# Kernel tuning notes

Hardware: AMD Instinct MI355X
Metric: run time of the kernel (lower is better)

Reference implementation:

```python
import jax, jax.numpy as jnp
import numpy as np

GROUPS = 8
EPS = 1e-5


def setup_inputs() -> dict:
    key = jax.random.key(0)
    ks = jax.random.split(key, 7)
    b, c, h, w = 32, 256, 32, 32
    x = jax.random.normal(ks[0], (b, c, h, w), dtype=jnp.float32)
    gn_weight = jax.random.normal(ks[1], (c,), dtype=jnp.float32) * 0.02 + 1.0
    gn_bias = jax.random.normal(ks[2], (c,), dtype=jnp.float32) * 0.02
    w_qkv = jax.random.normal(ks[3], (3 * c, c), dtype=jnp.float32) / np.sqrt(c)
    b_qkv = jax.random.normal(ks[4], (3 * c,), dtype=jnp.float32) * 0.01
    w_out = jax.random.normal(ks[5], (c, c), dtype=jnp.float32) / np.sqrt(c)
    b_out = jax.random.normal(ks[6], (c,), dtype=jnp.float32) * 0.01
    return {"x": x, "gn_weight": gn_weight, "gn_bias": gn_bias,
            "w_qkv": w_qkv, "b_qkv": b_qkv, "w_out": w_out, "b_out": b_out}


def group_norm(x, weight, bias):
    b, c, h, w = x.shape
    xg = x.reshape(b, GROUPS, c // GROUPS, h, w)
    mean = jnp.mean(xg, axis=(2, 3, 4), keepdims=True)
    var = jnp.var(xg, axis=(2, 3, 4), keepdims=True)
    xg = (xg - mean) * jax.lax.rsqrt(var + EPS)
    x = xg.reshape(b, c, h, w)
    return x * weight[None, :, None, None] + bias[None, :, None, None]


def reference(x, gn_weight, gn_bias, w_qkv, b_qkv, w_out, b_out):
    b, c, h, w = x.shape
    x_norm = group_norm(x, gn_weight, gn_bias)
    # 1x1 conv == channel matmul: (b, 3c, h, w)
    qkv = jnp.einsum('oc,bchw->bohw', w_qkv, x_norm) + b_qkv[None, :, None, None]
    q, k, v = jnp.split(qkv, 3, axis=1)
    hw = h * w
    q = q.reshape(b, c, hw)  # used transposed: (b, hw, c)
    k = k.reshape(b, c, hw)
    v = v.reshape(b, c, hw)
    scale = 1.0 / jnp.sqrt(jnp.float32(c))
    attn = jax.nn.softmax(jnp.einsum('bcs,bct->bst', q, k) * scale, axis=-1)  # (b, hw, hw)
    out = jnp.einsum('bst,bct->bcs', attn, v).reshape(b, c, h, w)
    out = jnp.einsum('oc,bchw->bohw', w_out, out) + b_out[None, :, None, None]
    return out + x
```

## Files before the change

kernel.cpp:

```cpp
#include <hip/hip_runtime.h>
#include <hip/hip_bf16.h>


typedef __bf16 bf16x8 __attribute__((ext_vector_type(8)));
typedef __bf16 bf16x4 __attribute__((ext_vector_type(4)));
typedef float f32x4 __attribute__((ext_vector_type(4)));
typedef float f32x16 __attribute__((ext_vector_type(16)));

#define MFMA16(a, b, c) __builtin_amdgcn_mfma_f32_16x16x32_bf16(a, b, c, 0, 0, 0)
#define MFMA32(a, b, c) __builtin_amdgcn_mfma_f32_32x32x16_bf16(a, b, c, 0, 0, 0)

#define GLD16(gsrc_, ldst_)                                                                  \
    __builtin_amdgcn_global_load_lds((const __attribute__((address_space(1))) void*)(gsrc_), \
                                     (__attribute__((address_space(3))) void*)(ldst_), 16, 0, 0)

__global__ __launch_bounds__(256) void gn_stats(const float* __restrict__ x,
                                                float* __restrict__ stats,
                                                const float* __restrict__ wqkv,
                                                const float* __restrict__ wout,
                                                __bf16* __restrict__ wbf) {
    const int bid = blockIdx.x, t = threadIdx.x;
    if (bid < 128) {
        int idx = (bid * 256 + t) * 8;
        const float* src = (idx < 196608) ? (wqkv + idx) : (wout + (idx - 196608));
        float4 v0 = *(const float4*)src;
        float4 v1 = *(const float4*)(src + 4);
        bf16x8 o;
        o[0] = (__bf16)v0.x; o[1] = (__bf16)v0.y; o[2] = (__bf16)v0.z; o[3] = (__bf16)v0.w;
        o[4] = (__bf16)v1.x; o[5] = (__bf16)v1.y; o[6] = (__bf16)v1.z; o[7] = (__bf16)v1.w;
        *(bf16x8*)&wbf[idx] = o;
    }
    const int bg = bid >> 3, part = bid & 7;
    const float* xp = x + (size_t)bg * 32768 + part * 4096;
    float s = 0.f, s2 = 0.f;
    #pragma unroll
    for (int i = 0; i < 4; i++) {
        float4 v = *(const float4*)(xp + (i * 256 + t) * 4);
        s  += v.x + v.y + v.z + v.w;
        s2 += v.x*v.x + v.y*v.y + v.z*v.z + v.w*v.w;
    }
    #pragma unroll
    for (int o = 32; o > 0; o >>= 1) { s += __shfl_down(s, o, 64); s2 += __shfl_down(s2, o, 64); }
    __shared__ float red[8];
    const int wv = t >> 6;
    if ((t & 63) == 0) { red[wv * 2] = s; red[wv * 2 + 1] = s2; }
    __syncthreads();
    if (t == 0) {
        float ts  = red[0] + red[2] + red[4] + red[6];
        float ts2 = red[1] + red[3] + red[5] + red[7];
        stats[bg * 16 + part * 2]     = ts;
        stats[bg * 16 + part * 2 + 1] = ts2;
    }
}

__global__ __launch_bounds__(512) void gn_apply(const float* __restrict__ x,
                                                const float* __restrict__ stats,
                                                const float* __restrict__ gw,
                                                const float* __restrict__ gb,
                                                __bf16* __restrict__ xnT) {
    const int bid = blockIdx.x;
    const int bg = bid >> 3, part = bid & 7;
    const int b = bg >> 3, g = bg & 7;
    const int t = threadIdx.x;
    float ts = 0.f, ts2 = 0.f;
    #pragma unroll
    for (int p = 0; p < 8; p++) { ts += stats[bg * 16 + p * 2]; ts2 += stats[bg * 16 + p * 2 + 1]; }
    const float mean = ts / 32768.f;
    const float inv = rsqrtf(ts2 / 32768.f - mean * mean + 1e-5f);
    __shared__ __bf16 Lds[32][136];
    const int c = t >> 4, ss = (t & 15) * 8;
    const float ga = gw[g * 32 + c], be = gb[g * 32 + c];
    const float* xp = x + (((size_t)b * 256 + g * 32 + c) * 1024) + part * 128 + ss;
    float4 v0 = *(const float4*)xp;
    float4 v1 = *(const float4*)(xp + 4);
    float vv[8] = {v0.x, v0.y, v0.z, v0.w, v1.x, v1.y, v1.z, v1.w};
    bf16x8 wv;
    #pragma unroll
    for (int i = 0; i < 8; i++) wv[i] = (__bf16)((vv[i] - mean) * inv * ga + be);
    *(bf16x8*)&Lds[c][ss] = wv;
    __syncthreads();
    const int row = t >> 2, cb = (t & 3) * 8;
    bf16x8 ov;
    #pragma unroll
    for (int j = 0; j < 8; j++) ov[j] = Lds[cb + j][row];
    *(bf16x8*)&xnT[((size_t)b * 1024 + part * 128 + row) * 256 + g * 32 + cb] = ov;
}

#define GEMM64P_BODY(ArowBase_, BrowBase_)                                              \
    f32x4 acc[4][4] = {};                                                               \
    {                                                                                   \
        _Pragma("unroll")                                                               \
        for (int i = 0; i < 4; i++) {                                                   \
            const int ch = wave * 4 + i;                                                \
            const int r = ch * 8 + (lane >> 3);                                         \
            const int sw = ((lane & 7) ^ (r & 7)) * 8;                                  \
            GLD16((ArowBase_) + (size_t)r * 256 + sw, (char*)&As[0][0][0] + ch * 1024); \
            GLD16((BrowBase_) + (size_t)r * 256 + sw, (char*)&Bs[0][0][0] + ch * 1024); \
        }                                                                               \
    }                                                                                   \
    _Pragma("unroll")                                                                   \
    for (int kk = 0; kk < 4; kk++) {                                                    \
        if (kk < 3) {                                                                   \
            _Pragma("unroll")                                                           \
            for (int i = 0; i < 4; i++) {                                               \
                const int ch = wave * 4 + i;                                            \
                const int r = ch * 8 + (lane >> 3);                                     \
                const int sw = ((lane & 7) ^ (r & 7)) * 8;                              \
                GLD16((ArowBase_) + (size_t)r * 256 + (kk + 1) * 64 + sw,               \
                      (char*)&As[(kk + 1) & 1][0][0] + ch * 1024);                      \
                GLD16((BrowBase_) + (size_t)r * 256 + (kk + 1) * 64 + sw,               \
                      (char*)&Bs[(kk + 1) & 1][0][0] + ch * 1024);                      \
            }                                                                           \
            asm volatile("s_waitcnt vmcnt(8)" ::: "memory");                            \
        } else {                                                                        \
            asm volatile("s_waitcnt vmcnt(0)" ::: "memory");                            \
        }                                                                               \
        asm volatile("s_barrier" ::: "memory");                                         \
        _Pragma("unroll")                                                               \
        for (int kh = 0; kh < 2; kh++) {                                                \
            bf16x8 af[4], bfv[4];                                                       \
            _Pragma("unroll")                                                           \
            for (int im = 0; im < 4; im++) {                                            \
                const int row = wm + im * 16 + l16;                                     \
                af[im] = *(const bf16x8*)&As[kk & 1][row][(((kh * 4 + quad) ^ (row & 7)) * 8)]; \
            }                                                                           \
            _Pragma("unroll")                                                           \
            for (int in = 0; in < 4; in++) {                                            \
                const int row = wn + in * 16 + l16;                                     \
                bfv[in] = *(const bf16x8*)&Bs[kk & 1][row][(((kh * 4 + quad) ^ (row & 7)) * 8)]; \
            }                                                                           \
            _Pragma("unroll")                                                           \
            for (int im = 0; im < 4; im++)                                              \
                _Pragma("unroll")                                                       \
                for (int in = 0; in < 4; in++)                                          \
                    acc[im][in] = MFMA16(af[im], bfv[in], acc[im][in]);                 \
        }                                                                               \
        asm volatile("s_waitcnt lgkmcnt(0)" ::: "memory");                              \
        asm volatile("s_barrier" ::: "memory");                                        \
    }

__global__ __launch_bounds__(256) void qkv_gemm(const __bf16* __restrict__ wbf,
                                                const float* __restrict__ bias,
                                                const __bf16* __restrict__ xnT,
                                                __bf16* __restrict__ qtr,
                                                __bf16* __restrict__ ktr,
                                                __bf16* __restrict__ vbuf) {
    __shared__ union {
        struct { __bf16 A[2][128][64]; __bf16 B[2][128][64]; } g;
        __bf16 ct[128][136];
    } sm;
    const int lin = blockIdx.x + ((blockIdx.y + blockIdx.z * 6) << 3);
    const int xcd = lin & 7, idx = lin >> 3;
    const int gwk = xcd * 192 + idx;
    const int mt = gwk % 6, panel = gwk / 6;
    const int b = panel >> 3;
    const int n0 = (panel & 7) * 128, m0 = mt * 128;
    const int t = threadIdx.x;
    const int wave = t >> 6, lane = t & 63, quad = lane >> 4, l16 = lane & 15;
    const int wm = (wave & 1) * 64, wn = (wave >> 1) * 64;
    const __bf16* arow = wbf + (size_t)m0 * 256;
    const __bf16* brow = xnT + ((size_t)b * 1024 + n0) * 256;
    auto As = sm.g.A;
    auto Bs = sm.g.B;

    GEMM64P_BODY(arow, brow)

    if (m0 < 512) {
        #pragma unroll
        for (int im = 0; im < 4; im++) {
            #pragma unroll
            for (int in = 0; in < 4; in++) {
                int ob = m0 + wm + im * 16 + quad * 4;
                bf16x4 ov;
                #pragma unroll
                for (int r = 0; r < 4; r++) ov[r] = (__bf16)(acc[im][in][r] + bias[ob + r]);
                *(bf16x4*)&sm.ct[wn + in * 16 + l16][wm + im * 16 + quad * 4] = ov;
            }
        }
        __syncthreads();
        {
            const int rbase = t >> 2, cf = t & 3;
            #pragma unroll
            for (int rr = 0; rr < 2; rr++) {
                int row = rbase + rr * 64;
                int sg = n0 + row;
                __bf16* dst = (m0 < 256) ? &qtr[((size_t)b * 1024 + sg) * 256 + m0]
                                         : &ktr[((size_t)b * 1024 + sg) * 256 + (m0 - 256)];
                #pragma unroll
                for (int u = 0; u < 4; u++) {
                    int colb = cf * 8 + u * 32;
                    *(bf16x8*)&dst[colb] = *(const bf16x8*)&sm.ct[row][colb];
                }
            }
        }
    } else {
        #pragma unroll
        for (int im = 0; im < 4; im++) {
            #pragma unroll
            for (int in = 0; in < 4; in++) {
                int cl = wm + im * 16 + quad * 4;
                int tl = wn + in * 16 + l16;
                #pragma unroll
                for (int r = 0; r < 4; r++)
                    sm.ct[cl + r][tl] = (__bf16)(acc[im][in][r] + bias[m0 + cl + r]);
            }
        }
        __syncthreads();
        {
            const int row = t >> 1, tc = (t & 1) * 64;
            const int cglob = m0 - 512 + row;
            __bf16* dst = &vbuf[((size_t)b * 256 + cglob) * 1024 + n0 + tc];
            #pragma unroll
            for (int u = 0; u < 8; u++)
                *(bf16x8*)&dst[u * 8] = *(const bf16x8*)&sm.ct[row][tc + u * 8];
        }
    }
}

__global__ __launch_bounds__(512, 2) void attn_kernel(const __bf16* __restrict__ qtr,
                                                      const __bf16* __restrict__ ktr,
                                                      const __bf16* __restrict__ vbuf,
                                                      __bf16* __restrict__ aoT) {
    __shared__ __bf16 Kt[2][32][260];
    __shared__ __bf16 Vs[2][256][36];
    __shared__ bf16x8 Pl[4][2][2][64];
    __shared__ float Lred[4][2][32];
    const int b = blockIdx.x;
    const int tid = threadIdx.x;
    const int wave = tid >> 6, lane = tid & 63, half = lane >> 5, l31 = lane & 31;
    const int pair = wave & 3, th = wave >> 2;
    const int s0 = blockIdx.y * 128 + pair * 32;
    const float kscale = 0.09016844f;

    bf16x8 aq[16];
    #pragma unroll
    for (int ks = 0; ks < 16; ks++)
        aq[ks] = *(const bf16x8*)&qtr[((size_t)b * 1024 + s0 + l31) * 256 + ks * 16 + half * 8];

    const int k_row = tid >> 3;
    const int k_cb  = (tid & 7) * 8;
    const int v_c   = tid >> 1;
    const int v_th  = tid & 1;
    const size_t kbase = (size_t)b * 1024 * 256;
    const size_t vbase = (size_t)b * 256 * 1024;

    float l_acc = 0.f;
    f32x16 o_acc[4] = {};

    bf16x8 kpre[4], vpre[4];
    #pragma unroll
    for (int u = 0; u < 4; u++) {
        kpre[u] = *(const bf16x8*)&ktr[kbase + (size_t)k_row * 256 + k_cb + u * 64];
        vpre[u] = *(const bf16x8*)&vbuf[vbase + (size_t)v_c * 1024 + v_th * 32 + u * 8];
    }

    for (int it = 0; it < 16; it++) {
        #pragma unroll
        for (int u = 0; u < 4; u++)
            *(bf16x8*)&Kt[k_row >> 5][k_row & 31][k_cb + u * 64] = kpre[u];
        #pragma unroll
        for (int u = 0; u < 4; u++) {
            const bf16x4* hv = (const bf16x4*)&vpre[u];
            const int sbase = (u >> 1) * 16 + (u & 1) * 4;
            *(bf16x4*)&Vs[v_th][v_c][sbase]     = hv[0];
            *(bf16x4*)&Vs[v_th][v_c][sbase + 8] = hv[1];
        }
        __syncthreads();
        if (it < 15) {
            const int t1 = (it + 1) * 64;
            #pragma unroll
            for (int u = 0; u < 4; u++) {
                kpre[u] = *(const bf16x8*)&ktr[kbase + (size_t)(t1 + k_row) * 256 + k_cb + u * 64];
                vpre[u] = *(const bf16x8*)&vbuf[vbase + (size_t)v_c * 1024 + t1 + v_th * 32 + u * 8];
            }
        }

        f32x16 sc_a = {}, sc_b = {};
        __builtin_amdgcn_s_setprio(1);
        #pragma unroll
        for (int ks = 0; ks < 8; ks++) {
            bf16x8 bk0 = *(const bf16x8*)&Kt[th][l31][ks * 16 + half * 8];
            bf16x8 bk1 = *(const bf16x8*)&Kt[th][l31][(ks + 8) * 16 + half * 8];
            sc_a = MFMA32(bk0, aq[ks], sc_a);
            sc_b = MFMA32(bk1, aq[ks + 8], sc_b);
        }
        __builtin_amdgcn_s_setprio(0);

        bf16x8 pf0, pf1;
        #pragma unroll
        for (int r = 0; r < 8; r++) {
            float p = exp2f((sc_a[r] + sc_b[r]) * kscale);
            l_acc += p;
            pf0[r] = (__bf16)p;
        }
        #pragma unroll
        for (int r = 8; r < 16; r++) {
            float p = exp2f((sc_a[r] + sc_b[r]) * kscale);
            l_acc += p;
            pf1[r - 8] = (__bf16)p;
        }
        Pl[pair][th][0][lane] = pf0;
        Pl[pair][th][1][lane] = pf1;
        __syncthreads();
        bf16x8 pp0 = Pl[pair][1 - th][0][lane];
        bf16x8 pp1 = Pl[pair][1 - th][1][lane];

        bf16x8 ap[4];
        if (th == 0) { ap[0] = pf0; ap[1] = pf1; ap[2] = pp0; ap[3] = pp1; }
        else         { ap[0] = pp0; ap[1] = pp1; ap[2] = pf0; ap[3] = pf1; }

        __builtin_amdgcn_s_setprio(1);
        #pragma unroll
        for (int n = 0; n < 4; n++) {
            int c = th * 128 + n * 32 + l31;
            #pragma unroll
            for (int kc = 0; kc < 4; kc++) {
                bf16x8 bv = *(const bf16x8*)&Vs[kc >> 1][c][(kc & 1) * 16 + half * 8];
                o_acc[n] = MFMA32(ap[kc], bv, o_acc[n]);
            }
        }
        __builtin_amdgcn_s_setprio(0);
        __syncthreads();
    }

    l_acc += __shfl_xor(l_acc, 32, 64);
    if (lane < 32) Lred[pair][th][l31] = l_acc;
    __syncthreads();
    #pragma unroll
    for (int r = 0; r < 16; r++) {
        int row = (r & 3) + 8 * (r >> 2) + 4 * half;
        float rinv = 1.0f / (Lred[pair][0][row] + Lred[pair][1][row]);
        #pragma unroll
        for (int n = 0; n < 4; n++) {
            int c = th * 128 + n * 32 + l31;
            aoT[((size_t)b * 1024 + s0 + row) * 256 + c] = (__bf16)(o_acc[n][r] * rinv);
        }
    }
}

__global__ __launch_bounds__(256) void proj_gemm(const __bf16* __restrict__ wbf_out,
                                                 const float* __restrict__ bias,
                                                 const __bf16* __restrict__ aoT,
                                                 const float* __restrict__ resid,
                                                 float* __restrict__ Out) {
    __shared__ union {
        struct { __bf16 A[2][128][64]; __bf16 B[2][128][64]; } g;
        float cf[64][132];
    } sm;
    const int lin = blockIdx.x + ((blockIdx.y + blockIdx.z * 2) << 3);
    const int xcd = lin & 7, idx = lin >> 3;
    const int gwk = xcd * 64 + idx;
    const int mt = gwk & 1, panel = gwk >> 1;
    const int b = panel >> 3;
    const int n0 = (panel & 7) * 128, m0 = mt * 128;
    const int t = threadIdx.x;
    const int wave = t >> 6, lane = t & 63, quad = lane >> 4, l16 = lane & 15;
    const int wm = (wave & 1) * 64, wn = (wave >> 1) * 64;
    const __bf16* arow = wbf_out + (size_t)m0 * 256;
    const __bf16* brow = aoT + ((size_t)b * 1024 + n0) * 256;
    auto As = sm.g.A;
    auto Bs = sm.g.B;

    GEMM64P_BODY(arow, brow)

    for (int h = 0; h < 2; h++) {
        if ((wave & 1) == h) {
            #pragma unroll
            for (int im = 0; im < 4; im++)
                #pragma unroll
                for (int in = 0; in < 4; in++)
                    #pragma unroll
                    for (int r = 0; r < 4; r++)
                        sm.cf[im * 16 + quad * 4 + r][wn + in * 16 + l16] = acc[im][in][r];
        }
        __syncthreads();
        {
            const int rloc = t >> 2, cq = (t & 3) * 4;
            const int o = m0 + h * 64 + rloc;
            const float bo = bias[o];
            const float* rrow = &resid[((size_t)b * 256 + o) * 1024 + n0];
            float* orow = &Out[((size_t)b * 256 + o) * 1024 + n0];
            #pragma unroll
            for (int u = 0; u < 8; u++) {
                int col = cq + u * 16;
                f32x4 cv = *(const f32x4*)&sm.cf[rloc][col];
                float4 rv = *(const float4*)&rrow[col];
                float4 ov;
                ov.x = cv[0] + bo + rv.x;
                ov.y = cv[1] + bo + rv.y;
                ov.z = cv[2] + bo + rv.z;
                ov.w = cv[3] + bo + rv.w;
                *(float4*)&orow[col] = ov;
            }
        }
        __syncthreads();
    }
}

extern "C" void kernel_launch(void* const* d_in, const int* in_sizes, int n_in,
                              void* d_out, int out_size, void* d_ws, size_t ws_size,
                              hipStream_t stream) {
    const float* x    = (const float*)d_in[0];
    const float* gw   = (const float*)d_in[1];
    const float* gb   = (const float*)d_in[2];
    const float* wqkv = (const float*)d_in[3];
    const float* bqkv = (const float*)d_in[4];
    const float* wout = (const float*)d_in[5];
    const float* bout = (const float*)d_in[6];
    float* out = (float*)d_out;

    const size_t T16 = (size_t)32 * 1024 * 256;
    __bf16* xnT  = (__bf16*)d_ws;
    __bf16* qtr  = xnT + T16;
    __bf16* ktr  = qtr + T16;
    __bf16* vbuf = ktr + T16;
    __bf16* aoT  = vbuf + T16;
    __bf16* wbf  = aoT + T16;
    float* gstats = (float*)(wbf + 262144);

    gn_stats<<<dim3(2048), 256, 0, stream>>>(x, gstats, wqkv, wout, wbf);
    gn_apply<<<dim3(2048), 512, 0, stream>>>(x, gstats, gw, gb, xnT);
    qkv_gemm<<<dim3(8, 6, 32), 256, 0, stream>>>(wbf, bqkv, xnT, qtr, ktr, vbuf);
    attn_kernel<<<dim3(32, 8), 512, 0, stream>>>(qtr, ktr, vbuf, aoT);
    proj_gemm<<<dim3(8, 2, 32), 256, 0, stream>>>(wbf + 196608, bout, aoT, x, out);
}
```

Baseline: 185.2 us.

## Fuse GroupNorm apply into QKV GEMM B-operand load from fp32 input

Measured after the change: 204.1 us. +10.2%, slower.

```diff
diff --git a/kernel.cpp b/kernel.cpp
--- a/kernel.cpp
+++ b/kernel.cpp
@@ -4,6 +4,7 @@
 
 typedef __bf16 bf16x8 __attribute__((ext_vector_type(8)));
 typedef __bf16 bf16x4 __attribute__((ext_vector_type(4)));
+typedef __bf16 bf16x2 __attribute__((ext_vector_type(2)));
 typedef float f32x4 __attribute__((ext_vector_type(4)));
 typedef float f32x16 __attribute__((ext_vector_type(16)));
 
@@ -53,37 +54,297 @@
     }
 }
 
-__global__ __launch_bounds__(512) void gn_apply(const float* __restrict__ x,
-                                                const float* __restrict__ stats,
+__global__ __launch_bounds__(256) void qkv_gemm(const __bf16* __restrict__ wbf,
+                                                const float* __restrict__ bias,
+                                                const float* __restrict__ x,
+                                                const float* __restrict__ gstats,
                                                 const float* __restrict__ gw,
                                                 const float* __restrict__ gb,
-                                                __bf16* __restrict__ xnT) {
-    const int bid = blockIdx.x;
-    const int bg = bid >> 3, part = bid & 7;
-    const int b = bg >> 3, g = bg & 7;
+                                                __bf16* __restrict__ qtr,
+                                                __bf16* __restrict__ ktr,
+                                                __bf16* __restrict__ vbuf) {
+    __shared__ union {
+        struct { __bf16 A[128][64]; __bf16 B[128][72]; } g;
+        __bf16 ct[128][136];
+    } sm;
+    __shared__ float sM[8], sI[8];
+    const int lin = blockIdx.x + ((blockIdx.y + blockIdx.z * 6) << 3);
+    const int xcd = lin & 7, idx = lin >> 3;
+    const int gwk = xcd * 192 + idx;
+    const int mt = gwk % 6, panel = gwk / 6;
+    const int b = panel >> 3;
+    const int n0 = (panel & 7) * 128, m0 = mt * 128;
     const int t = threadIdx.x;
-    float ts = 0.f, ts2 = 0.f;
+    const int wave = t >> 6, lane = t & 63, quad = lane >> 4, l16 = lane & 15;
+    const int wm = (wave & 1) * 64, wn = (wave >> 1) * 64;
+    const __bf16* arow = wbf + (size_t)m0 * 256;
+    auto As = sm.g.A;
+    auto Bs = sm.g.B;
+
+    if (t < 128) {
+        const int g = t >> 4, j = t & 15;
+        float v = gstats[((size_t)b * 8 + g) * 16 + j];
+        v += __shfl_xor(v, 2, 64);
+        v += __shfl_xor(v, 4, 64);
+        v += __shfl_xor(v, 8, 64);
+        float w = __shfl_xor(v, 1, 64);
+        if (j == 0) {
+            float mean = v / 32768.f;
+            sM[g] = mean;
+            sI[g] = rsqrtf(w / 32768.f - mean * mean + 1e-5f);
+        }
+    }
+    __syncthreads();
+
+    const int cl = (t & 31) * 2;
+    const int sh = t >> 5;
+    float bpre[32];
+    float nsc0, nof0, nsc1, nof1;
+
+#define PREFETCH_B(KC_)                                                                 \
+    {                                                                                   \
+        const int ch = (KC_) + cl;                                                      \
+        const int gg = ch >> 5;                                                         \
+        const float* xb = x + (((size_t)b * 256 + ch) * 1024) + n0 + sh * 16;           \
+        _Pragma("unroll")                                                               \
+        for (int u = 0; u < 4; u++) *(float4*)&bpre[u * 4] = *(const float4*)(xb + u * 4); \
+        _Pragma("unroll")                                                               \
+        for (int u = 0; u < 4; u++) *(float4*)&bpre[16 + u * 4] = *(const float4*)(xb + 1024 + u * 4); \
+        float m_ = sM[gg], iv_ = sI[gg];                                                \
+        nsc0 = iv_ * gw[ch];     nof0 = gb[ch]     - m_ * nsc0;                         \
+        nsc1 = iv_ * gw[ch + 1]; nof1 = gb[ch + 1] - m_ * nsc1;                         \
+    }
+
+#define WRITE_B()                                                                       \
+    {                                                                                   \
+        _Pragma("unroll")                                                               \
+        for (int i = 0; i < 16; i++) {                                                  \
+            bf16x2 e;                                                                   \
+            e[0] = (__bf16)(bpre[i] * nsc0 + nof0);                                     \
+            e[1] = (__bf16)(bpre[16 + i] * nsc1 + nof1);                                \
+            *(bf16x2*)&Bs[sh * 16 + i][cl] = e;                                         \
+        }                                                                               \
+    }
+
+#define GLD_A(KC_)                                                                      \
+    {                                                                                   \
+        _Pragma("unroll")                                                               \
+        for (int i = 0; i < 4; i++) {                                                   \
+            const int ch_ = wave * 4 + i;                                               \
+            const int r_ = ch_ * 8 + (lane >> 3);                                       \
+            const int sw_ = ((lane & 7) ^ (r_ & 7)) * 8;                                \
+            GLD16(arow + (size_t)r_ * 256 + (KC_) + sw_, (char*)&As[0][0] + ch_ * 1024); \
+        }                                                                               \
+    }
+
+    f32x4 acc[4][4] = {};
+
+    PREFETCH_B(0)
+    GLD_A(0)
+    WRITE_B()
+    __syncthreads();
+
+    for (int kk = 0; kk < 4; kk++) {
+        if (kk < 3) PREFETCH_B((kk + 1) * 64)
+        #pragma unroll
+        for (int kh = 0; kh < 2; kh++) {
+            bf16x8 af[4], bfv[4];
+            #pragma unroll
+            for (int im = 0; im < 4; im++) {
+                const int row = wm + im * 16 + l16;
+                af[im] = *(const bf16x8*)&As[row][(((kh * 4 + quad) ^ (row & 7)) * 8)];
+            }
+            #pragma unroll
+            for (int in = 0; in < 4; in++)
+                bfv[in] = *(const bf16x8*)&Bs[wn + in * 16 + l16][kh * 32 + quad * 8];
+            #pragma unroll
+            for (int im = 0; im < 4; im++)
+                #pragma unroll
+                for (int in = 0; in < 4; in++)
+                    acc[im][in] = MFMA16(af[im], bfv[in], acc[im][in]);
+        }
+        __syncthreads();
+        if (kk < 3) {
+            GLD_A((kk + 1) * 64)
+            WRITE_B()
+            __syncthreads();
+        }
+    }
+#undef PREFETCH_B
+#undef WRITE_B
+#undef GLD_A
+
+    if (m0 < 512) {
+        #pragma unroll
+        for (int im = 0; im < 4; im++) {
+            #pragma unroll
+            for (int in = 0; in < 4; in++) {
+                int ob = m0 + wm + im * 16 + quad * 4;
+                bf16x4 ov;
+                #pragma unroll
+                for (int r = 0; r < 4; r++) ov[r] = (__bf16)(acc[im][in][r] + bias[ob + r]);
+                *(bf16x4*)&sm.ct[wn + in * 16 + l16][wm + im * 16 + quad * 4] = ov;
+            }
+        }
+        __syncthreads();
+        {
+            const int rbase = t >> 2, cf = t & 3;
+            #pragma unroll
+            for (int rr = 0; rr < 2; rr++) {
+                int row = rbase + rr * 64;
+                int sg = n0 + row;
+                __bf16* dst = (m0 < 256) ? &qtr[((size_t)b * 1024 + sg) * 256 + m0]
+                                         : &ktr[((size_t)b * 1024 + sg) * 256 + (m0 - 256)];
+                #pragma unroll
+                for (int u = 0; u < 4; u++) {
+                    int colb = cf * 8 + u * 32;
+                    *(bf16x8*)&dst[colb] = *(const bf16x8*)&sm.ct[row][colb];
+                }
+            }
+        }
+    } else {
+        #pragma unroll
+        for (int im = 0; im < 4; im++) {
+            #pragma unroll
+            for (int in = 0; in < 4; in++) {
+                int cc = wm + im * 16 + quad * 4;
+                int tl = wn + in * 16 + l16;
+                #pragma unroll
+                for (int r = 0; r < 4; r++)
+                    sm.ct[cc + r][tl] = (__bf16)(acc[im][in][r] + bias[m0 + cc + r]);
+            }
+        }
+        __syncthreads();
+        {
+            const int row = t >> 1, tc = (t & 1) * 64;
+            const int cglob = m0 - 512 + row;
+            __bf16* dst = &vbuf[((size_t)b * 256 + cglob) * 1024 + n0 + tc];
+            #pragma unroll
+            for (int u = 0; u < 8; u++)
+                *(bf16x8*)&dst[u * 8] = *(const bf16x8*)&sm.ct[row][tc + u * 8];
+        }
+    }
+}
+
+__global__ __launch_bounds__(512, 2) void attn_kernel(const __bf16* __restrict__ qtr,
+                                                      const __bf16* __restrict__ ktr,
+                                                      const __bf16* __restrict__ vbuf,
+                                                      __bf16* __restrict__ aoT) {
+    __shared__ __bf16 Kt[2][32][260];
+    __shared__ __bf16 Vs[2][256][36];
+    __shared__ bf16x8 Pl[4][2][2][64];
+    __shared__ float Lred[4][2][32];
+    const int b = blockIdx.x;
+    const int tid = threadIdx.x;
+    const int wave = tid >> 6, lane = tid & 63, half = lane >> 5, l31 = lane & 31;
+    const int pair = wave & 3, th = wave >> 2;
+    const int s0 = blockIdx.y * 128 + pair * 32;
+    const float kscale = 0.09016844f;
+
+    bf16x8 aq[16];
     #pragma unroll
-    for (int p = 0; p < 8; p++) { ts += stats[bg * 16 + p * 2]; ts2 += stats[bg * 16 + p * 2 + 1]; }
-    const float mean = ts / 32768.f;
-    const float inv = rsqrtf(ts2 / 32768.f - mean * mean + 1e-5f);
-    __shared__ __bf16 Lds[32][136];
-    const int c = t >> 4, ss = (t & 15) * 8;
-    const float ga = gw[g * 32 + c], be = gb[g * 32 + c];
-    const float* xp = x + (((size_t)b * 256 + g * 32 + c) * 1024) + part * 128 + ss;
-    float4 v0 = *(const float4*)xp;
-    float4 v1 = *(const float4*)(xp + 4);
-    float vv[8] = {v0.x, v0.y, v0.z, v0.w, v1.x, v1.y, v1.z, v1.w};
-    bf16x8 wv;
+    for (int ks = 0; ks < 16; ks++)
+        aq[ks] = *(const bf16x8*)&qtr[((size_t)b * 1024 + s0 + l31) * 256 + ks * 16 + half * 8];
+
+    const int k_row = tid >> 3;
+    const int k_cb  = (tid & 7) * 8;
+    const int v_c   = tid >> 1;
+    const int v_th  = tid & 1;
+    const size_t kbase = (size_t)b * 1024 * 256;
+    const size_t vbase = (size_t)b * 256 * 1024;
+
+    float l_acc = 0.f;
+    f32x16 o_acc[4] = {};
+
+    bf16x8 kpre[4], vpre[4];
     #pragma unroll
-    for (int i = 0; i < 8; i++) wv[i] = (__bf16)((vv[i] - mean) * inv * ga + be);
-    *(bf16x8*)&Lds[c][ss] = wv;
+    for (int u = 0; u < 4; u++) {
+        kpre[u] = *(const bf16x8*)&ktr[kbase + (size_t)k_row * 256 + k_cb + u * 64];
+        vpre[u] = *(const bf16x8*)&vbuf[vbase + (size_t)v_c * 1024 + v_th * 32 + u * 8];
+    }
+
+    for (int it = 0; it < 16; it++) {
+        #pragma unroll
+        for (int u = 0; u < 4; u++)
+            *(bf16x8*)&Kt[k_row >> 5][k_row & 31][k_cb + u * 64] = kpre[u];
+        #pragma unroll
+        for (int u = 0; u < 4; u++) {
+            const bf16x4* hv = (const bf16x4*)&vpre[u];
+            const int sbase = (u >> 1) * 16 + (u & 1) * 4;
+            *(bf16x4*)&Vs[v_th][v_c][sbase]     = hv[0];
+            *(bf16x4*)&Vs[v_th][v_c][sbase + 8] = hv[1];
+        }
+        __syncthreads();
+        if (it < 15) {
+            const int t1 = (it + 1) * 64;
+            #pragma unroll
+            for (int u = 0; u < 4; u++) {
+                kpre[u] = *(const bf16x8*)&ktr[kbase + (size_t)(t1 + k_row) * 256 + k_cb + u * 64];
+                vpre[u] = *(const bf16x8*)&vbuf[vbase + (size_t)v_c * 1024 + t1 + v_th * 32 + u * 8];
+            }
+        }
+
+        f32x16 sc_a = {}, sc_b = {};
+        __builtin_amdgcn_s_setprio(1);
+        #pragma unroll
+        for (int ks = 0; ks < 8; ks++) {
+            bf16x8 bk0 = *(const bf16x8*)&Kt[th][l31][ks * 16 + half * 8];
+            bf16x8 bk1 = *(const bf16x8*)&Kt[th][l31][(ks + 8) * 16 + half * 8];
+            sc_a = MFMA32(bk0, aq[ks], sc_a);
+            sc_b = MFMA32(bk1, aq[ks + 8], sc_b);
+        }
+        __builtin_amdgcn_s_setprio(0);
+
+        bf16x8 pf0, pf1;
+        #pragma unroll
+        for (int r = 0; r < 8; r++) {
+            float p = exp2f((sc_a[r] + sc_b[r]) * kscale);
+            l_acc += p;
+            pf0[r] = (__bf16)p;
+        }
+        #pragma unroll
+        for (int r = 8; r < 16; r++) {
+            float p = exp2f((sc_a[r] + sc_b[r]) * kscale);
+            l_acc += p;
+            pf1[r - 8] = (__bf16)p;
+        }
+        Pl[pair][th][0][lane] = pf0;
+        Pl[pair][th][1][lane] = pf1;
+        __syncthreads();
+        bf16x8 pp0 = Pl[pair][1 - th][0][lane];
+        bf16x8 pp1 = Pl[pair][1 - th][1][lane];
+
+        bf16x8 ap[4];
+        if (th == 0) { ap[0] = pf0; ap[1] = pf1; ap[2] = pp0; ap[3] = pp1; }
+        else         { ap[0] = pp0; ap[1] = pp1; ap[2] = pf0; ap[3] = pf1; }
+
+        __builtin_amdgcn_s_setprio(1);
+        #pragma unroll
+        for (int n = 0; n < 4; n++) {
+            int c = th * 128 + n * 32 + l31;
+            #pragma unroll
+            for (int kc = 0; kc < 4; kc++) {
+                bf16x8 bv = *(const bf16x8*)&Vs[kc >> 1][c][(kc & 1) * 16 + half * 8];
+                o_acc[n] = MFMA32(ap[kc], bv, o_acc[n]);
+            }
+        }
+        __builtin_amdgcn_s_setprio(0);
+        __syncthreads();
+    }
+
+    l_acc += __shfl_xor(l_acc, 32, 64);
+    if (lane < 32) Lred[pair][th][l31] = l_acc;
     __syncthreads();
-    const int row = t >> 2, cb = (t & 3) * 8;
-    bf16x8 ov;
     #pragma unroll
-    for (int j = 0; j < 8; j++) ov[j] = Lds[cb + j][row];
-    *(bf16x8*)&xnT[((size_t)b * 1024 + part * 128 + row) * 256 + g * 32 + cb] = ov;
+    for (int r = 0; r < 16; r++) {
+        int row = (r & 3) + 8 * (r >> 2) + 4 * half;
+        float rinv = 1.0f / (Lred[pair][0][row] + Lred[pair][1][row]);
+        #pragma unroll
+        for (int n = 0; n < 4; n++) {
+            int c = th * 128 + n * 32 + l31;
+            aoT[((size_t)b * 1024 + s0 + row) * 256 + c] = (__bf16)(o_acc[n][r] * rinv);
+        }
+    }
 }
 
 #define GEMM64P_BODY(ArowBase_, BrowBase_)                                              \
@@ -139,205 +400,6 @@
         asm volatile("s_barrier" ::: "memory");                                        \
     }
 
-__global__ __launch_bounds__(256) void qkv_gemm(const __bf16* __restrict__ wbf,
-                                                const float* __restrict__ bias,
-                                                const __bf16* __restrict__ xnT,
-                                                __bf16* __restrict__ qtr,
-                                                __bf16* __restrict__ ktr,
-                                                __bf16* __restrict__ vbuf) {
-    __shared__ union {
-        struct { __bf16 A[2][128][64]; __bf16 B[2][128][64]; } g;
-        __bf16 ct[128][136];
-    } sm;
-    const int lin = blockIdx.x + ((blockIdx.y + blockIdx.z * 6) << 3);
-    const int xcd = lin & 7, idx = lin >> 3;
-    const int gwk = xcd * 192 + idx;
-    const int mt = gwk % 6, panel = gwk / 6;
-    const int b = panel >> 3;
-    const int n0 = (panel & 7) * 128, m0 = mt * 128;
-    const int t = threadIdx.x;
-    const int wave = t >> 6, lane = t & 63, quad = lane >> 4, l16 = lane & 15;
-    const int wm = (wave & 1) * 64, wn = (wave >> 1) * 64;
-    const __bf16* arow = wbf + (size_t)m0 * 256;
-    const __bf16* brow = xnT + ((size_t)b * 1024 + n0) * 256;
-    auto As = sm.g.A;
-    auto Bs = sm.g.B;
-
-    GEMM64P_BODY(arow, brow)
-
-    if (m0 < 512) {
-        #pragma unroll
-        for (int im = 0; im < 4; im++) {
-            #pragma unroll
-            for (int in = 0; in < 4; in++) {
-                int ob = m0 + wm + im * 16 + quad * 4;
-                bf16x4 ov;
-                #pragma unroll
-                for (int r = 0; r < 4; r++) ov[r] = (__bf16)(acc[im][in][r] + bias[ob + r]);
-                *(bf16x4*)&sm.ct[wn + in * 16 + l16][wm + im * 16 + quad * 4] = ov;
-            }
-        }
-        __syncthreads();
-        {
-            const int rbase = t >> 2, cf = t & 3;
-            #pragma unroll
-            for (int rr = 0; rr < 2; rr++) {
-                int row = rbase + rr * 64;
-                int sg = n0 + row;
-                __bf16* dst = (m0 < 256) ? &qtr[((size_t)b * 1024 + sg) * 256 + m0]
-                                         : &ktr[((size_t)b * 1024 + sg) * 256 + (m0 - 256)];
-                #pragma unroll
-                for (int u = 0; u < 4; u++) {
-                    int colb = cf * 8 + u * 32;
-                    *(bf16x8*)&dst[colb] = *(const bf16x8*)&sm.ct[row][colb];
-                }
-            }
-        }
-    } else {
-        #pragma unroll
-        for (int im = 0; im < 4; im++) {
-            #pragma unroll
-            for (int in = 0; in < 4; in++) {
-                int cl = wm + im * 16 + quad * 4;
-                int tl = wn + in * 16 + l16;
-                #pragma unroll
-                for (int r = 0; r < 4; r++)
-                    sm.ct[cl + r][tl] = (__bf16)(acc[im][in][r] + bias[m0 + cl + r]);
-            }
-        }
-        __syncthreads();
-        {
-            const int row = t >> 1, tc = (t & 1) * 64;
-            const int cglob = m0 - 512 + row;
-            __bf16* dst = &vbuf[((size_t)b * 256 + cglob) * 1024 + n0 + tc];
-            #pragma unroll
-            for (int u = 0; u < 8; u++)
-                *(bf16x8*)&dst[u * 8] = *(const bf16x8*)&sm.ct[row][tc + u * 8];
-        }
-    }
-}
-
-__global__ __launch_bounds__(512, 2) void attn_kernel(const __bf16* __restrict__ qtr,
-                                                      const __bf16* __restrict__ ktr,
-                                                      const __bf16* __restrict__ vbuf,
-                                                      __bf16* __restrict__ aoT) {
-    __shared__ __bf16 Kt[2][32][260];
-    __shared__ __bf16 Vs[2][256][36];
-    __shared__ bf16x8 Pl[4][2][2][64];
-    __shared__ float Lred[4][2][32];
-    const int b = blockIdx.x;
-    const int tid = threadIdx.x;
-    const int wave = tid >> 6, lane = tid & 63, half = lane >> 5, l31 = lane & 31;
-    const int pair = wave & 3, th = wave >> 2;
-    const int s0 = blockIdx.y * 128 + pair * 32;
-    const float kscale = 0.09016844f;
-
-    bf16x8 aq[16];
-    #pragma unroll
-    for (int ks = 0; ks < 16; ks++)
-        aq[ks] = *(const bf16x8*)&qtr[((size_t)b * 1024 + s0 + l31) * 256 + ks * 16 + half * 8];
-
-    const int k_row = tid >> 3;
-    const int k_cb  = (tid & 7) * 8;
-    const int v_c   = tid >> 1;
-    const int v_th  = tid & 1;
-    const size_t kbase = (size_t)b * 1024 * 256;
-    const size_t vbase = (size_t)b * 256 * 1024;
-
-    float l_acc = 0.f;
-    f32x16 o_acc[4] = {};
-
-    bf16x8 kpre[4], vpre[4];
-    #pragma unroll
-    for (int u = 0; u < 4; u++) {
-        kpre[u] = *(const bf16x8*)&ktr[kbase + (size_t)k_row * 256 + k_cb + u * 64];
-        vpre[u] = *(const bf16x8*)&vbuf[vbase + (size_t)v_c * 1024 + v_th * 32 + u * 8];
-    }
-
-    for (int it = 0; it < 16; it++) {
-        #pragma unroll
-        for (int u = 0; u < 4; u++)
-            *(bf16x8*)&Kt[k_row >> 5][k_row & 31][k_cb + u * 64] = kpre[u];
-        #pragma unroll
-        for (int u = 0; u < 4; u++) {
-            const bf16x4* hv = (const bf16x4*)&vpre[u];
-            const int sbase = (u >> 1) * 16 + (u & 1) * 4;
-            *(bf16x4*)&Vs[v_th][v_c][sbase]     = hv[0];
-            *(bf16x4*)&Vs[v_th][v_c][sbase + 8] = hv[1];
-        }
-        __syncthreads();
-        if (it < 15) {
-            const int t1 = (it + 1) * 64;
-            #pragma unroll
-            for (int u = 0; u < 4; u++) {
-                kpre[u] = *(const bf16x8*)&ktr[kbase + (size_t)(t1 + k_row) * 256 + k_cb + u * 64];
-                vpre[u] = *(const bf16x8*)&vbuf[vbase + (size_t)v_c * 1024 + t1 + v_th * 32 + u * 8];
-            }
-        }
-
-        f32x16 sc_a = {}, sc_b = {};
-        __builtin_amdgcn_s_setprio(1);
-        #pragma unroll
-        for (int ks = 0; ks < 8; ks++) {
-            bf16x8 bk0 = *(const bf16x8*)&Kt[th][l31][ks * 16 + half * 8];
-            bf16x8 bk1 = *(const bf16x8*)&Kt[th][l31][(ks + 8) * 16 + half * 8];
-            sc_a = MFMA32(bk0, aq[ks], sc_a);
-            sc_b = MFMA32(bk1, aq[ks + 8], sc_b);
-        }
-        __builtin_amdgcn_s_setprio(0);
-
-        bf16x8 pf0, pf1;
-        #pragma unroll
-        for (int r = 0; r < 8; r++) {
-            float p = exp2f((sc_a[r] + sc_b[r]) * kscale);
-            l_acc += p;
-            pf0[r] = (__bf16)p;
-        }
-        #pragma unroll
-        for (int r = 8; r < 16; r++) {
-            float p = exp2f((sc_a[r] + sc_b[r]) * kscale);
-            l_acc += p;
-            pf1[r - 8] = (__bf16)p;
-        }
-        Pl[pair][th][0][lane] = pf0;
-        Pl[pair][th][1][lane] = pf1;
-        __syncthreads();
-        bf16x8 pp0 = Pl[pair][1 - th][0][lane];
-        bf16x8 pp1 = Pl[pair][1 - th][1][lane];
-
-        bf16x8 ap[4];
-        if (th == 0) { ap[0] = pf0; ap[1] = pf1; ap[2] = pp0; ap[3] = pp1; }
-        else         { ap[0] = pp0; ap[1] = pp1; ap[2] = pf0; ap[3] = pf1; }
-
-        __builtin_amdgcn_s_setprio(1);
-        #pragma unroll
-        for (int n = 0; n < 4; n++) {
-            int c = th * 128 + n * 32 + l31;
-            #pragma unroll
-            for (int kc = 0; kc < 4; kc++) {
-                bf16x8 bv = *(const bf16x8*)&Vs[kc >> 1][c][(kc & 1) * 16 + half * 8];
-                o_acc[n] = MFMA32(ap[kc], bv, o_acc[n]);
-            }
-        }
-        __builtin_amdgcn_s_setprio(0);
-        __syncthreads();
-    }
-
-    l_acc += __shfl_xor(l_acc, 32, 64);
-    if (lane < 32) Lred[pair][th][l31] = l_acc;
-    __syncthreads();
-    #pragma unroll
-    for (int r = 0; r < 16; r++) {
-        int row = (r & 3) + 8 * (r >> 2) + 4 * half;
-        float rinv = 1.0f / (Lred[pair][0][row] + Lred[pair][1][row]);
-        #pragma unroll
-        for (int n = 0; n < 4; n++) {
-            int c = th * 128 + n * 32 + l31;
-            aoT[((size_t)b * 1024 + s0 + row) * 256 + c] = (__bf16)(o_acc[n][r] * rinv);
-        }
-    }
-}
-
 __global__ __launch_bounds__(256) void proj_gemm(const __bf16* __restrict__ wbf_out,
                                                  const float* __restrict__ bias,
                                                  const __bf16* __restrict__ aoT,
@@ -419,8 +481,7 @@
     float* gstats = (float*)(wbf + 262144);
 
     gn_stats<<<dim3(2048), 256, 0, stream>>>(x, gstats, wqkv, wout, wbf);
-    gn_apply<<<dim3(2048), 512, 0, stream>>>(x, gstats, gw, gb, xnT);
-    qkv_gemm<<<dim3(8, 6, 32), 256, 0, stream>>>(wbf, bqkv, xnT, qtr, ktr, vbuf);
+    qkv_gemm<<<dim3(8, 6, 32), 256, 0, stream>>>(wbf, bqkv, x, gstats, gw, gb, qtr, ktr, vbuf);
     attn_kernel<<<dim3(32, 8), 512, 0, stream>>>(qtr, ktr, vbuf, aoT);
     proj_gemm<<<dim3(8, 2, 32), 256, 0, stream>>>(wbf + 196608, bout, aoT, x, out);
 }
```
